# Performance work log

Hardware: AMD Instinct MI355X
Metric: run time of the kernel (lower is better)

## Reference

```python
import jax, jax.numpy as jnp
import numpy as np

EPS = 1e-5

def _layer_norm(x, gamma, beta):
    mu = jnp.mean(x, axis=-1, keepdims=True)
    var = jnp.var(x, axis=-1, keepdims=True)
    return (x - mu) * jax.lax.rsqrt(var + EPS) * gamma + beta

def setup_inputs() -> dict:
    key = jax.random.key(0)
    ks = jax.random.split(key, 4)
    B, T, D, H = 16, 2048, 1024, 1024
    s_in = 1.0 / np.sqrt(D)
    return {
        "x": jax.random.normal(ks[0], (B, T, D), dtype=jnp.float32),
        "c": jnp.zeros((B, H), dtype=jnp.float32),
        "W_lt": jax.random.uniform(ks[1], (H, D), jnp.float32, -s_in, s_in),
        "W_g": jax.random.uniform(ks[2], (2 * H, D), jnp.float32, -s_in, s_in),
        "b_g": jnp.zeros((2 * H,), dtype=jnp.float32),
        "gamma_g": jnp.ones((2 * H,), dtype=jnp.float32),
        "beta_g": jnp.zeros((2 * H,), dtype=jnp.float32),
        "gamma_a": jnp.ones((H,), dtype=jnp.float32),
        "beta_a": jnp.zeros((H,), dtype=jnp.float32),
    }

def reference(x, c, W_lt, W_g, b_g, gamma_g, beta_g, gamma_a, beta_a):
    H = W_lt.shape[0]
    # x: [B,T,D]
    x_tilde = jnp.einsum("btd,hd->bth", x, W_lt)            # [B,T,H]
    gate = jax.nn.sigmoid(_layer_norm(jnp.einsum("btd,gd->btg", x, W_g) + b_g, gamma_g, beta_g))
    f = gate[:, :, :H]                                        # forget gate [B,T,H]
    r = gate[:, :, H:]                                        # reset gate  [B,T,H]
    new_data = (1.0 - f) * x_tilde

    def step(c_prev, ft_nd):
        f_t, nd_t = ft_nd
        c_t = f_t * c_prev + nd_t
        return c_t, c_t

    # scan over time: move T to leading axis
    c_final, all_c = jax.lax.scan(step, c, (jnp.swapaxes(f, 0, 1), jnp.swapaxes(new_data, 0, 1)))
    all_c = jnp.swapaxes(all_c, 0, 1)                         # [B,T,H]
    h = r * jax.nn.sigmoid(_layer_norm(all_c, gamma_a, beta_a)) + (1.0 - r) * x
    return (h, c_final)
```

## Files before the change

### kernel.cpp

```cpp
#include <hip/hip_runtime.h>
#include <stdint.h>

typedef unsigned short u16;
typedef u16 us8 __attribute__((ext_vector_type(8)));
typedef uint32_t u32x8 __attribute__((ext_vector_type(8)));
typedef __bf16 bf16x8 __attribute__((ext_vector_type(8)));
typedef float f32x4 __attribute__((ext_vector_type(4)));

#define BB 16
#define TT 2048
#define HH 1024
#define MM 32768
#define NN 3072
#define KK 1024
#define NT 16

__device__ __forceinline__ float b2f(u16 u) {
    union { uint32_t i; float f; } v; v.i = ((uint32_t)u) << 16; return v.f;
}
__device__ __forceinline__ u16 f2b(float f) {
    union { uint32_t i; float f; } v; v.f = f;
    uint32_t r = v.i + 0x7fffu + ((v.i >> 16) & 1u);
    return (u16)(r >> 16);
}
__device__ __forceinline__ float sigm(float z) {
    return 1.f / (1.f + __expf(-z));
}
__device__ __forceinline__ void load_lds16(const u16* g, u16* l) {
    __builtin_amdgcn_global_load_lds(
        (const __attribute__((address_space(1))) void*)g,
        (__attribute__((address_space(3))) void*)l, 16, 0, 0);
}
__device__ __forceinline__ f32x4 mf(bf16x8 a, bf16x8 b, f32x4 c) {
    return __builtin_amdgcn_mfma_f32_16x16x32_bf16(a, b, c, 0, 0, 0);
}
#define MEMBAR() asm volatile("" ::: "memory")

__global__ __launch_bounds__(256) void k_cvt(const float* __restrict__ x,
                                             const float* __restrict__ wlt,
                                             const float* __restrict__ wg,
                                             u16* __restrict__ xb,
                                             u16* __restrict__ wb) {
    long i = (long)(blockIdx.x * 256 + threadIdx.x) * 8;
    const float* s;
    u16* o;
    if (i < 33554432L) { s = x + i; o = xb + i; }
    else {
        long j = i - 33554432L;
        s = (j < 1048576L) ? (wlt + j) : (wg + (j - 1048576L));
        o = wb + j;
    }
    float4 a = *(const float4*)(s);
    float4 b = *(const float4*)(s + 4);
    us8 r;
    r[0] = f2b(a.x); r[1] = f2b(a.y); r[2] = f2b(a.z); r[3] = f2b(a.w);
    r[4] = f2b(b.x); r[5] = f2b(b.y); r[6] = f2b(b.z); r[7] = f2b(b.w);
    *(us8*)o = r;
}

__global__ __launch_bounds__(512, 2) void k_gemm(const u16* __restrict__ A,
                                                 const u16* __restrict__ W,
                                                 u16* __restrict__ Y) {
    __shared__ u16 As[2 * 16384];
    __shared__ u16 Bs[2 * 16384];
    const int tid = threadIdx.x;
    const int lane = tid & 63;
    const int w = tid >> 6;
    const int wm = w >> 2;
    const int wn = w & 3;
    const int q = lane >> 4;
    const int l16 = lane & 15;

    const unsigned bid = blockIdx.y * 12u + blockIdx.x;
    const unsigned sw = (bid & 7u) * 192u + (bid >> 3);
    const int by = sw / 12u;
    const int bx = sw % 12u;

    const int slog = ((tid & 7) ^ ((tid >> 3) & 7)) << 3;
    const u16* aS = A + (size_t)(by * 256 + (tid >> 3)) * KK + slog;
    const u16* bS = W + (size_t)(bx * 256 + ((tid >> 8) << 6) + ((tid >> 3) & 31)) * KK + slog;
    u16* aD = As + w * 512;
    u16* bD = Bs + w * 512;

    load_lds16(aS,                aD);
    load_lds16(aS + 128 * KK,     aD + 4096);
    load_lds16(aS + 64 * KK,      aD + 8192);
    load_lds16(aS + 192 * KK,     aD + 12288);
    load_lds16(bS,                bD);
    load_lds16(bS + 128 * KK,     bD + 4096);
    load_lds16(bS + 32 * KK,      bD + 8192);
    load_lds16(bS + 160 * KK,     bD + 12288);
    load_lds16(aS + 64,           aD + 16384);
    load_lds16(aS + 64 + 128*KK,  aD + 16384 + 4096);
    load_lds16(aS + 64 + 64*KK,   aD + 16384 + 8192);
    load_lds16(aS + 64 + 192*KK,  aD + 16384 + 12288);
    load_lds16(bS + 64,           bD + 16384);
    load_lds16(bS + 64 + 128*KK,  bD + 16384 + 4096);
    load_lds16(bS + 64 + 32*KK,   bD + 16384 + 8192);
    load_lds16(bS + 64 + 160*KK,  bD + 16384 + 12288);

    const int key = l16 & 7;
    const int sA0 = ((q ^ key) << 3);
    const int sA1 = (((q ^ key) ^ 4) << 3);
    const int aB0 = wm * 4096 + l16 * 64 + sA0;
    const int aB1 = wm * 4096 + l16 * 64 + sA1;
    const int bB0 = wn * 2048 + l16 * 64 + sA0;
    const int bB1 = wn * 2048 + l16 * 64 + sA1;

    f32x4 zero = {0.f, 0.f, 0.f, 0.f};
    f32x4 acc[8][4];
#pragma unroll
    for (int i = 0; i < 8; ++i)
#pragma unroll
        for (int j = 0; j < 4; ++j) acc[i][j] = zero;
    bf16x8 aX[4], aY[4], bLo[4], bHi[4];

    asm volatile("s_waitcnt vmcnt(8)" ::: "memory");
    __builtin_amdgcn_sched_barrier(0);
    __builtin_amdgcn_s_barrier();
    MEMBAR();

    for (int kt = 0; kt < NT - 1; ++kt) {
        const int cb = (kt & 1) << 14;
        const int kc = (kt + 2) << 6;
        const bool st = (kt < NT - 2);
#pragma unroll
        for (int i = 0; i < 4; ++i) {
            aX[i] = *(const bf16x8*)&As[cb + i * 1024 + aB0];
            aY[i] = *(const bf16x8*)&As[cb + i * 1024 + aB1];
        }
        bLo[0] = *(const bf16x8*)&Bs[cb + bB0];
        bLo[1] = *(const bf16x8*)&Bs[cb + bB1];
        bLo[2] = *(const bf16x8*)&Bs[cb + 1024 + bB0];
        bLo[3] = *(const bf16x8*)&Bs[cb + 1024 + bB1];
        asm volatile("s_waitcnt lgkmcnt(8)" ::: "memory");
        __builtin_amdgcn_sched_barrier(0);
        __builtin_amdgcn_s_barrier();
        asm volatile("s_waitcnt lgkmcnt(0)" ::: "memory");
        __builtin_amdgcn_sched_barrier(0);
        __builtin_amdgcn_s_setprio(1);
#pragma unroll
        for (int i = 0; i < 4; ++i) {
            acc[i][0] = mf(aX[i], bLo[0], acc[i][0]);
            acc[i][0] = mf(aY[i], bLo[1], acc[i][0]);
            acc[i][1] = mf(aX[i], bLo[2], acc[i][1]);
            acc[i][1] = mf(aY[i], bLo[3], acc[i][1]);
        }
        __builtin_amdgcn_s_setprio(0);
        MEMBAR();
        __builtin_amdgcn_s_barrier();
        MEMBAR();
        bHi[0] = *(const bf16x8*)&Bs[cb + 8192 + bB0];
        bHi[1] = *(const bf16x8*)&Bs[cb + 8192 + bB1];
        bHi[2] = *(const bf16x8*)&Bs[cb + 8192 + 1024 + bB0];
        bHi[3] = *(const bf16x8*)&Bs[cb + 8192 + 1024 + bB1];
        if (st) {
            load_lds16(aS + kc,            aD + cb);
            load_lds16(aS + kc + 128*KK,   aD + cb + 4096);
            load_lds16(bS + kc,            bD + cb);
            load_lds16(bS + kc + 128*KK,   bD + cb + 4096);
        }
        __builtin_amdgcn_sched_barrier(0);
        __builtin_amdgcn_s_barrier();
        asm volatile("s_waitcnt lgkmcnt(0)" ::: "memory");
        __builtin_amdgcn_sched_barrier(0);
        __builtin_amdgcn_s_setprio(1);
#pragma unroll
        for (int i = 0; i < 4; ++i) {
            acc[i][2] = mf(aX[i], bHi[0], acc[i][2]);
            acc[i][2] = mf(aY[i], bHi[1], acc[i][2]);
            acc[i][3] = mf(aX[i], bHi[2], acc[i][3]);
            acc[i][3] = mf(aY[i], bHi[3], acc[i][3]);
        }
        __builtin_amdgcn_s_setprio(0);
        MEMBAR();
        __builtin_amdgcn_s_barrier();
        MEMBAR();
#pragma unroll
        for (int i = 0; i < 4; ++i) {
            aX[i] = *(const bf16x8*)&As[cb + 8192 + i * 1024 + aB0];
            aY[i] = *(const bf16x8*)&As[cb + 8192 + i * 1024 + aB1];
        }
        if (st) {
            load_lds16(bS + kc + 32*KK,    bD + cb + 8192);
            load_lds16(bS + kc + 160*KK,   bD + cb + 12288);
        }
        __builtin_amdgcn_sched_barrier(0);
        __builtin_amdgcn_s_barrier();
        asm volatile("s_waitcnt lgkmcnt(0)" ::: "memory");
        __builtin_amdgcn_sched_barrier(0);
        __builtin_amdgcn_s_setprio(1);
#pragma unroll
        for (int i = 0; i < 4; ++i) {
            acc[4 + i][0] = mf(aX[i], bLo[0], acc[4 + i][0]);
            acc[4 + i][0] = mf(aY[i], bLo[1], acc[4 + i][0]);
            acc[4 + i][1] = mf(aX[i], bLo[2], acc[4 + i][1]);
            acc[4 + i][1] = mf(aY[i], bLo[3], acc[4 + i][1]);
        }
        __builtin_amdgcn_s_setprio(0);
        MEMBAR();
        __builtin_amdgcn_s_barrier();
        MEMBAR();
        if (st) {
            load_lds16(aS + kc + 64*KK,    aD + cb + 8192);
            load_lds16(aS + kc + 192*KK,   aD + cb + 12288);
        }
        __builtin_amdgcn_sched_barrier(0);
        __builtin_amdgcn_s_barrier();
        __builtin_amdgcn_s_setprio(1);
#pragma unroll
        for (int i = 0; i < 4; ++i) {
            acc[4 + i][2] = mf(aX[i], bHi[0], acc[4 + i][2]);
            acc[4 + i][2] = mf(aY[i], bHi[1], acc[4 + i][2]);
            acc[4 + i][3] = mf(aX[i], bHi[2], acc[4 + i][3]);
            acc[4 + i][3] = mf(aY[i], bHi[3], acc[4 + i][3]);
        }
        __builtin_amdgcn_s_setprio(0);
        if (st) { asm volatile("s_waitcnt vmcnt(8)" ::: "memory"); }
        else    { asm volatile("s_waitcnt vmcnt(0)" ::: "memory"); }
        __builtin_amdgcn_sched_barrier(0);
        __builtin_amdgcn_s_barrier();
        MEMBAR();
    }

    {
        const int cb = 16384;
#pragma unroll
        for (int i = 0; i < 4; ++i) {
            aX[i] = *(const bf16x8*)&As[cb + i * 1024 + aB0];
            aY[i] = *(const bf16x8*)&As[cb + i * 1024 + aB1];
        }
        bLo[0] = *(const bf16x8*)&Bs[cb + bB0];
        bLo[1] = *(const bf16x8*)&Bs[cb + bB1];
        bLo[2] = *(const bf16x8*)&Bs[cb + 1024 + bB0];
        bLo[3] = *(const bf16x8*)&Bs[cb + 1024 + bB1];
        bHi[0] = *(const bf16x8*)&Bs[cb + 8192 + bB0];
        bHi[1] = *(const bf16x8*)&Bs[cb + 8192 + bB1];
        bHi[2] = *(const bf16x8*)&Bs[cb + 8192 + 1024 + bB0];
        bHi[3] = *(const bf16x8*)&Bs[cb + 8192 + 1024 + bB1];
#pragma unroll
        for (int i = 0; i < 4; ++i) {
            acc[i][0] = mf(aX[i], bLo[0], acc[i][0]);
            acc[i][0] = mf(aY[i], bLo[1], acc[i][0]);
            acc[i][1] = mf(aX[i], bLo[2], acc[i][1]);
            acc[i][1] = mf(aY[i], bLo[3], acc[i][1]);
            acc[i][2] = mf(aX[i], bHi[0], acc[i][2]);
            acc[i][2] = mf(aY[i], bHi[1], acc[i][2]);
            acc[i][3] = mf(aX[i], bHi[2], acc[i][3]);
            acc[i][3] = mf(aY[i], bHi[3], acc[i][3]);
        }
#pragma unroll
        for (int i = 0; i < 4; ++i) {
            aX[i] = *(const bf16x8*)&As[cb + 8192 + i * 1024 + aB0];
            aY[i] = *(const bf16x8*)&As[cb + 8192 + i * 1024 + aB1];
        }
#pragma unroll
        for (int i = 0; i < 4; ++i) {
            acc[4 + i][0] = mf(aX[i], bLo[0], acc[4 + i][0]);
            acc[4 + i][0] = mf(aY[i], bLo[1], acc[4 + i][0]);
            acc[4 + i][1] = mf(aX[i], bLo[2], acc[4 + i][1]);
            acc[4 + i][1] = mf(aY[i], bLo[3], acc[4 + i][1]);
            acc[4 + i][2] = mf(aX[i], bHi[0], acc[4 + i][2]);
            acc[4 + i][2] = mf(aY[i], bHi[1], acc[4 + i][2]);
            acc[4 + i][3] = mf(aX[i], bHi[2], acc[4 + i][3]);
            acc[4 + i][3] = mf(aY[i], bHi[3], acc[4 + i][3]);
        }
    }

#pragma unroll
    for (int fm = 0; fm < 8; ++fm) {
#pragma unroll
        for (int rg = 0; rg < 4; ++rg) {
            const int row = by * 256 + wm * 128 + fm * 16 + q * 4 + rg;
            u16* yp = Y + (size_t)row * NN + bx * 256 + wn * 64 + l16;
#pragma unroll
            for (int fn = 0; fn < 4; ++fn) yp[fn * 16] = f2b(acc[fm][fn][rg]);
        }
    }
}

__global__ __launch_bounds__(256) void k_lnsig(const u16* __restrict__ Y,
                                               const float* __restrict__ bg,
                                               const float* __restrict__ gg,
                                               const float* __restrict__ bt,
                                               uint32_t* __restrict__ FN,
                                               u16* __restrict__ R) {
    const int row = blockIdx.x;
    const int t = threadIdx.x;
    const u16* yr = Y + (size_t)row * 3072;
    us8 gv = *(const us8*)(yr + 1024 + t * 8);
    us8 xt;
    if (t < 128) xt = *(const us8*)(yr + t * 8);
    float z[8];
    float s = 0.f, s2 = 0.f;
#pragma unroll
    for (int k = 0; k < 8; k++) {
        z[k] = b2f(gv[k]) + bg[t * 8 + k];
        s += z[k];
        s2 += z[k] * z[k];
    }
#pragma unroll
    for (int m = 1; m < 64; m <<= 1) {
        s += __shfl_xor(s, m);
        s2 += __shfl_xor(s2, m);
    }
    __shared__ float red[8];
    if ((t & 63) == 0) { red[t >> 6] = s; red[(t >> 6) + 4] = s2; }
    asm volatile("s_waitcnt lgkmcnt(0)" ::: "memory");
    __builtin_amdgcn_sched_barrier(0);
    __builtin_amdgcn_s_barrier();
    MEMBAR();
    s = red[0] + red[1] + red[2] + red[3];
    s2 = red[4] + red[5] + red[6] + red[7];
    const float mu = s * (1.f / 2048.f);
    const float inv = rsqrtf(s2 * (1.f / 2048.f) - mu * mu + 1e-5f);
    float gate[8];
#pragma unroll
    for (int k = 0; k < 8; k++)
        gate[k] = sigm((z[k] - mu) * inv * gg[t * 8 + k] + bt[t * 8 + k]);
    if (t < 128) {
        u32x8 fn;
#pragma unroll
        for (int k = 0; k < 8; k++) {
            u16 fb = f2b(gate[k]);
            u16 nb = f2b((1.f - gate[k]) * b2f(xt[k]));
            fn[k] = (uint32_t)fb | ((uint32_t)nb << 16);
        }
        *(u32x8*)(FN + (size_t)row * 1024 + t * 8) = fn;
    } else {
        us8 ro;
#pragma unroll
        for (int k = 0; k < 8; k++) ro[k] = f2b(gate[k]);
        *(us8*)(R + (size_t)row * 1024 + (t - 128) * 8) = ro;
    }
}

__global__ __launch_bounds__(256) void k_scan1(const uint32_t* __restrict__ FN,
                                               float2* __restrict__ agg) {
    int u = blockIdx.x * 256 + threadIdx.x;
    int h2 = u & 511;
    int chunk = (u >> 9) & 31;
    int b = u >> 14;
    size_t base = (size_t)(b * 2048 + chunk * 64) * 1024 + h2 * 2;
    float F0 = 1.f, N0 = 0.f, F1 = 1.f, N1 = 0.f;
#pragma unroll 8
    for (int i = 0; i < 64; i++) {
        uint2 v = *(const uint2*)(FN + base + (size_t)i * 1024);
        float f0 = b2f((u16)(v.x & 0xffffu)), n0 = b2f((u16)(v.x >> 16));
        float f1 = b2f((u16)(v.y & 0xffffu)), n1 = b2f((u16)(v.y >> 16));
        N0 = fmaf(f0, N0, n0); F0 *= f0;
        N1 = fmaf(f1, N1, n1); F1 *= f1;
    }
    float4 o = {F0, N0, F1, N1};
    *(float4*)&agg[(size_t)(b * 32 + chunk) * 1024 + h2 * 2] = o;
}

__global__ __launch_bounds__(256) void k_scan2(const float2* __restrict__ agg,
                                               const float* __restrict__ c0,
                                               float* __restrict__ P) {
    int u = blockIdx.x * 256 + threadIdx.x;
    int b = u >> 10, h = u & 1023;
    float c = c0[u];
#pragma unroll 8
    for (int k = 0; k < 32; k++) {
        size_t idx = (size_t)(b * 32 + k) * 1024 + h;
        P[idx] = c;
        float2 fn = agg[idx];
        c = fmaf(fn.x, c, fn.y);
    }
}

#define SOUT_STEP(fnv, rvv, xvv, ro, p)                                        \
    {                                                                          \
        c0 = fmaf(b2f((u16)((fnv).x & 0xffffu)), c0, b2f((u16)((fnv).x >> 16)));\
        c1 = fmaf(b2f((u16)((fnv).y & 0xffffu)), c1, b2f((u16)((fnv).y >> 16)));\
        float s = c0 + c1, s2 = c0 * c0 + c1 * c1;                             \
        _Pragma("unroll")                                                      \
        for (int m = 1; m < 64; m <<= 1) {                                     \
            s += __shfl_xor(s, m);                                             \
            s2 += __shfl_xor(s2, m);                                           \
        }                                                                      \
        if (lane == 0) red[p][w] = make_float2(s, s2);                         \
        asm volatile("s_waitcnt lgkmcnt(0)" ::: "memory");                     \
        __builtin_amdgcn_sched_barrier(0);                                     \
        __builtin_amdgcn_s_barrier();                                          \
        MEMBAR();                                                              \
        s = 0.f; s2 = 0.f;                                                     \
        _Pragma("unroll")                                                      \
        for (int k = 0; k < 8; k++) { float2 v = red[p][k]; s += v.x; s2 += v.y; } \
        const float mu = s * (1.f / 1024.f);                                   \
        const float inv = rsqrtf(s2 * (1.f / 1024.f) - mu * mu + 1e-5f);       \
        const float sg0 = sigm((c0 - mu) * inv * g0 + be0);                    \
        const float sg1 = sigm((c1 - mu) * inv * g1 + be1);                    \
        const float r0 = b2f((u16)((rvv) & 0xffffu)), r1 = b2f((u16)((rvv) >> 16)); \
        const float x0 = b2f((u16)((xvv) & 0xffffu)), x1 = b2f((u16)((xvv) >> 16)); \
        float2 ho = {r0 * sg0 + (1.f - r0) * x0, r1 * sg1 + (1.f - r1) * x1};  \
        *(float2*)(out + (ro)) = ho;                                           \
    }

__global__ __launch_bounds__(512) void k_scanout(const uint32_t* __restrict__ FN,
                                                 const float* __restrict__ P,
                                                 const u16* __restrict__ R,
                                                 const u16* __restrict__ xb,
                                                 const float* __restrict__ ga,
                                                 const float* __restrict__ ba,
                                                 float* __restrict__ out,
                                                 float* __restrict__ cfin) {
    __shared__ float2 red[2][8];
    const int t = threadIdx.x;
    const int b = blockIdx.x >> 5, chunk = blockIdx.x & 31;
    const int h = t * 2;
    const int w = t >> 6, lane = t & 63;
    float2 cp = *(const float2*)&P[(size_t)(b * 32 + chunk) * 1024 + h];
    float c0 = cp.x, c1 = cp.y;
    const float g0 = ga[h], g1 = ga[h + 1];
    const float be0 = ba[h], be1 = ba[h + 1];
    const size_t base = (size_t)(b * 2048 + chunk * 64) * 1024 + h;

    uint2 fnA = *(const uint2*)(FN + base);
    uint32_t rvA = *(const uint32_t*)(R + base);
    uint32_t xvA = *(const uint32_t*)(xb + base);
    uint2 fnB = *(const uint2*)(FN + base + 1024);
    uint32_t rvB = *(const uint32_t*)(R + base + 1024);
    uint32_t xvB = *(const uint32_t*)(xb + base + 1024);

    for (int ii = 0; ii < 32; ++ii) {
        const size_t ro0 = base + (size_t)(2 * ii) * 1024;
        {
            uint2 fn = fnA; uint32_t rv = rvA, xv = xvA;
            if (ii < 31) {
                const size_t rn = ro0 + 2048;
                fnA = *(const uint2*)(FN + rn);
                rvA = *(const uint32_t*)(R + rn);
                xvA = *(const uint32_t*)(xb + rn);
            }
            SOUT_STEP(fn, rv, xv, ro0, 0)
        }
        {
            uint2 fn = fnB; uint32_t rv = rvB, xv = xvB;
            if (ii < 31) {
                const size_t rn = ro0 + 3072;
                fnB = *(const uint2*)(FN + rn);
                rvB = *(const uint32_t*)(R + rn);
                xvB = *(const uint32_t*)(xb + rn);
            }
            SOUT_STEP(fn, rv, xv, ro0 + 1024, 1)
        }
    }
    if (chunk == 31) *(float2*)(cfin + b * 1024 + h) = make_float2(c0, c1);
}

extern "C" void kernel_launch(void* const* d_in, const int* in_sizes, int n_in,
                              void* d_out, int out_size, void* d_ws, size_t ws_size,
                              hipStream_t stream) {
    const float* x   = (const float*)d_in[0];
    const float* c0  = (const float*)d_in[1];
    const float* wlt = (const float*)d_in[2];
    const float* wg  = (const float*)d_in[3];
    const float* bg  = (const float*)d_in[4];
    const float* gg  = (const float*)d_in[5];
    const float* btg = (const float*)d_in[6];
    const float* ga  = (const float*)d_in[7];
    const float* ba  = (const float*)d_in[8];
    float* out = (float*)d_out;

    char* ws = (char*)d_ws;
    u16* xb      = (u16*)(ws);
    u16* wb      = (u16*)(ws + 67108864);
    u16* y       = (u16*)(ws + 73400320);
    uint32_t* FN = (uint32_t*)(ws + 274726912);
    u16* R       = (u16*)(ws + 408944640);
    float2* agg  = (float2*)(ws + 476053504);
    float* P     = (float*)(ws + 480247808);

    k_cvt<<<17920, 256, 0, stream>>>(x, wlt, wg, xb, wb);
    k_gemm<<<dim3(NN / 256, MM / 256), 512, 0, stream>>>(xb, wb, y);
    k_lnsig<<<32768, 256, 0, stream>>>(y, bg, gg, btg, FN, R);
    k_scan1<<<1024, 256, 0, stream>>>(FN, agg);
    k_scan2<<<64, 256, 0, stream>>>(agg, c0, P);
    k_scanout<<<512, 512, 0, stream>>>(FN, P, R, xb, ga, ba, out,
                                       out + (size_t)33554432);
}
```

Baseline: 632.3 us.

## Make layernorm and scan-output kernels wave-per-row and shorten scan chunks

The LN+sigmoid kernel now gives each 64-lane wave a full row, so it no longer needs the shared-memory block reduction and barrier. The scan is split into 128 chunks of 16 steps instead of 32 chunks of 64. The output kernel has each wave own one (batch, chunk) unit across all 1024 channels, which removes the per-timestep block barrier and leaves only wave shuffles. Agg and P move to reuse the dead GEMM output region, and k_scan2 now runs a longer serial chain of 128 steps.

```diff
diff --git a/kernel.cpp b/kernel.cpp
--- a/kernel.cpp
+++ b/kernel.cpp
@@ -285,53 +285,64 @@
                                                const float* __restrict__ bt,
                                                uint32_t* __restrict__ FN,
                                                u16* __restrict__ R) {
-    const int row = blockIdx.x;
-    const int t = threadIdx.x;
+    const int lane = threadIdx.x & 63;
+    const int row = blockIdx.x * 4 + (threadIdx.x >> 6);
     const u16* yr = Y + (size_t)row * 3072;
-    us8 gv = *(const us8*)(yr + 1024 + t * 8);
-    us8 xt;
-    if (t < 128) xt = *(const us8*)(yr + t * 8);
-    float z[8];
+    const int g0i = 8 * lane;
+    us8 gv[4];
+    us8 xt[2];
+#pragma unroll
+    for (int j = 0; j < 4; ++j) gv[j] = *(const us8*)(yr + 1024 + g0i + 512 * j);
+#pragma unroll
+    for (int j = 0; j < 2; ++j) xt[j] = *(const us8*)(yr + g0i + 512 * j);
+    float z[4][8];
     float s = 0.f, s2 = 0.f;
 #pragma unroll
-    for (int k = 0; k < 8; k++) {
-        z[k] = b2f(gv[k]) + bg[t * 8 + k];
-        s += z[k];
-        s2 += z[k] * z[k];
+    for (int j = 0; j < 4; ++j) {
+        const float4 ba_ = *(const float4*)(bg + g0i + 512 * j);
+        const float4 bb_ = *(const float4*)(bg + g0i + 512 * j + 4);
+#pragma unroll
+        for (int k = 0; k < 4; ++k) {
+            z[j][k]     = b2f(gv[j][k])     + ((const float*)&ba_)[k];
+            z[j][k + 4] = b2f(gv[j][k + 4]) + ((const float*)&bb_)[k];
+        }
+#pragma unroll
+        for (int k = 0; k < 8; ++k) { s += z[j][k]; s2 = fmaf(z[j][k], z[j][k], s2); }
     }
 #pragma unroll
     for (int m = 1; m < 64; m <<= 1) {
         s += __shfl_xor(s, m);
         s2 += __shfl_xor(s2, m);
     }
-    __shared__ float red[8];
-    if ((t & 63) == 0) { red[t >> 6] = s; red[(t >> 6) + 4] = s2; }
-    asm volatile("s_waitcnt lgkmcnt(0)" ::: "memory");
-    __builtin_amdgcn_sched_barrier(0);
-    __builtin_amdgcn_s_barrier();
-    MEMBAR();
-    s = red[0] + red[1] + red[2] + red[3];
-    s2 = red[4] + red[5] + red[6] + red[7];
     const float mu = s * (1.f / 2048.f);
     const float inv = rsqrtf(s2 * (1.f / 2048.f) - mu * mu + 1e-5f);
-    float gate[8];
-#pragma unroll
-    for (int k = 0; k < 8; k++)
-        gate[k] = sigm((z[k] - mu) * inv * gg[t * 8 + k] + bt[t * 8 + k]);
-    if (t < 128) {
-        u32x8 fn;
-#pragma unroll
-        for (int k = 0; k < 8; k++) {
-            u16 fb = f2b(gate[k]);
-            u16 nb = f2b((1.f - gate[k]) * b2f(xt[k]));
-            fn[k] = (uint32_t)fb | ((uint32_t)nb << 16);
-        }
-        *(u32x8*)(FN + (size_t)row * 1024 + t * 8) = fn;
-    } else {
-        us8 ro;
-#pragma unroll
-        for (int k = 0; k < 8; k++) ro[k] = f2b(gate[k]);
-        *(us8*)(R + (size_t)row * 1024 + (t - 128) * 8) = ro;
+#pragma unroll
+    for (int j = 0; j < 4; ++j) {
+        const float4 ga_ = *(const float4*)(gg + g0i + 512 * j);
+        const float4 gb_ = *(const float4*)(gg + g0i + 512 * j + 4);
+        const float4 ta_ = *(const float4*)(bt + g0i + 512 * j);
+        const float4 tb_ = *(const float4*)(bt + g0i + 512 * j + 4);
+        float gate[8];
+#pragma unroll
+        for (int k = 0; k < 4; ++k) {
+            gate[k]     = sigm((z[j][k] - mu) * inv * ((const float*)&ga_)[k] + ((const float*)&ta_)[k]);
+            gate[k + 4] = sigm((z[j][k + 4] - mu) * inv * ((const float*)&gb_)[k] + ((const float*)&tb_)[k]);
+        }
+        if (j < 2) {
+            u32x8 fn;
+#pragma unroll
+            for (int k = 0; k < 8; ++k) {
+                u16 fb = f2b(gate[k]);
+                u16 nb = f2b((1.f - gate[k]) * b2f(xt[j][k]));
+                fn[k] = (uint32_t)fb | ((uint32_t)nb << 16);
+            }
+            *(u32x8*)(FN + (size_t)row * 1024 + g0i + 512 * j) = fn;
+        } else {
+            us8 ro;
+#pragma unroll
+            for (int k = 0; k < 8; ++k) ro[k] = f2b(gate[k]);
+            *(us8*)(R + (size_t)row * 1024 + g0i + 512 * (j - 2)) = ro;
+        }
     }
 }
 
@@ -339,12 +350,12 @@
                                                float2* __restrict__ agg) {
     int u = blockIdx.x * 256 + threadIdx.x;
     int h2 = u & 511;
-    int chunk = (u >> 9) & 31;
-    int b = u >> 14;
-    size_t base = (size_t)(b * 2048 + chunk * 64) * 1024 + h2 * 2;
+    int chunk = (u >> 9) & 127;
+    int b = u >> 16;
+    size_t base = (size_t)(b * 2048 + chunk * 16) * 1024 + h2 * 2;
     float F0 = 1.f, N0 = 0.f, F1 = 1.f, N1 = 0.f;
-#pragma unroll 8
-    for (int i = 0; i < 64; i++) {
+#pragma unroll
+    for (int i = 0; i < 16; i++) {
         uint2 v = *(const uint2*)(FN + base + (size_t)i * 1024);
         float f0 = b2f((u16)(v.x & 0xffffu)), n0 = b2f((u16)(v.x >> 16));
         float f1 = b2f((u16)(v.y & 0xffffu)), n1 = b2f((u16)(v.y >> 16));
@@ -352,7 +363,7 @@
         N1 = fmaf(f1, N1, n1); F1 *= f1;
     }
     float4 o = {F0, N0, F1, N1};
-    *(float4*)&agg[(size_t)(b * 32 + chunk) * 1024 + h2 * 2] = o;
+    *(float4*)&agg[(size_t)(b * 128 + chunk) * 1024 + h2 * 2] = o;
 }
 
 __global__ __launch_bounds__(256) void k_scan2(const float2* __restrict__ agg,
@@ -361,44 +372,16 @@
     int u = blockIdx.x * 256 + threadIdx.x;
     int b = u >> 10, h = u & 1023;
     float c = c0[u];
-#pragma unroll 8
-    for (int k = 0; k < 32; k++) {
-        size_t idx = (size_t)(b * 32 + k) * 1024 + h;
+#pragma unroll 4
+    for (int k = 0; k < 128; k++) {
+        size_t idx = (size_t)(b * 128 + k) * 1024 + h;
         P[idx] = c;
         float2 fn = agg[idx];
         c = fmaf(fn.x, c, fn.y);
     }
 }
 
-#define SOUT_STEP(fnv, rvv, xvv, ro, p)                                        \
-    {                                                                          \
-        c0 = fmaf(b2f((u16)((fnv).x & 0xffffu)), c0, b2f((u16)((fnv).x >> 16)));\
-        c1 = fmaf(b2f((u16)((fnv).y & 0xffffu)), c1, b2f((u16)((fnv).y >> 16)));\
-        float s = c0 + c1, s2 = c0 * c0 + c1 * c1;                             \
-        _Pragma("unroll")                                                      \
-        for (int m = 1; m < 64; m <<= 1) {                                     \
-            s += __shfl_xor(s, m);                                             \
-            s2 += __shfl_xor(s2, m);                                           \
-        }                                                                      \
-        if (lane == 0) red[p][w] = make_float2(s, s2);                         \
-        asm volatile("s_waitcnt lgkmcnt(0)" ::: "memory");                     \
-        __builtin_amdgcn_sched_barrier(0);                                     \
-        __builtin_amdgcn_s_barrier();                                          \
-        MEMBAR();                                                              \
-        s = 0.f; s2 = 0.f;                                                     \
-        _Pragma("unroll")                                                      \
-        for (int k = 0; k < 8; k++) { float2 v = red[p][k]; s += v.x; s2 += v.y; } \
-        const float mu = s * (1.f / 1024.f);                                   \
-        const float inv = rsqrtf(s2 * (1.f / 1024.f) - mu * mu + 1e-5f);       \
-        const float sg0 = sigm((c0 - mu) * inv * g0 + be0);                    \
-        const float sg1 = sigm((c1 - mu) * inv * g1 + be1);                    \
-        const float r0 = b2f((u16)((rvv) & 0xffffu)), r1 = b2f((u16)((rvv) >> 16)); \
-        const float x0 = b2f((u16)((xvv) & 0xffffu)), x1 = b2f((u16)((xvv) >> 16)); \
-        float2 ho = {r0 * sg0 + (1.f - r0) * x0, r1 * sg1 + (1.f - r1) * x1};  \
-        *(float2*)(out + (ro)) = ho;                                           \
-    }
-
-__global__ __launch_bounds__(512) void k_scanout(const uint32_t* __restrict__ FN,
+__global__ __launch_bounds__(256) void k_scanout(const uint32_t* __restrict__ FN,
                                                  const float* __restrict__ P,
                                                  const u16* __restrict__ R,
                                                  const u16* __restrict__ xb,
@@ -406,48 +389,63 @@
                                                  const float* __restrict__ ba,
                                                  float* __restrict__ out,
                                                  float* __restrict__ cfin) {
-    __shared__ float2 red[2][8];
-    const int t = threadIdx.x;
-    const int b = blockIdx.x >> 5, chunk = blockIdx.x & 31;
-    const int h = t * 2;
-    const int w = t >> 6, lane = t & 63;
-    float2 cp = *(const float2*)&P[(size_t)(b * 32 + chunk) * 1024 + h];
-    float c0 = cp.x, c1 = cp.y;
-    const float g0 = ga[h], g1 = ga[h + 1];
-    const float be0 = ba[h], be1 = ba[h + 1];
-    const size_t base = (size_t)(b * 2048 + chunk * 64) * 1024 + h;
-
-    uint2 fnA = *(const uint2*)(FN + base);
-    uint32_t rvA = *(const uint32_t*)(R + base);
-    uint32_t xvA = *(const uint32_t*)(xb + base);
-    uint2 fnB = *(const uint2*)(FN + base + 1024);
-    uint32_t rvB = *(const uint32_t*)(R + base + 1024);
-    uint32_t xvB = *(const uint32_t*)(xb + base + 1024);
-
-    for (int ii = 0; ii < 32; ++ii) {
-        const size_t ro0 = base + (size_t)(2 * ii) * 1024;
-        {
-            uint2 fn = fnA; uint32_t rv = rvA, xv = xvA;
-            if (ii < 31) {
-                const size_t rn = ro0 + 2048;
-                fnA = *(const uint2*)(FN + rn);
-                rvA = *(const uint32_t*)(R + rn);
-                xvA = *(const uint32_t*)(xb + rn);
-            }
-            SOUT_STEP(fn, rv, xv, ro0, 0)
-        }
-        {
-            uint2 fn = fnB; uint32_t rv = rvB, xv = xvB;
-            if (ii < 31) {
-                const size_t rn = ro0 + 3072;
-                fnB = *(const uint2*)(FN + rn);
-                rvB = *(const uint32_t*)(R + rn);
-                xvB = *(const uint32_t*)(xb + rn);
-            }
-            SOUT_STEP(fn, rv, xv, ro0 + 1024, 1)
-        }
-    }
-    if (chunk == 31) *(float2*)(cfin + b * 1024 + h) = make_float2(c0, c1);
+    const int lane = threadIdx.x & 63;
+    const int unit = blockIdx.x * 4 + (threadIdx.x >> 6);
+    const int b = unit >> 7, chunk = unit & 127;
+    float c0[8], c1[8], gg0[8], gg1[8], bb0[8], bb1[8];
+    const size_t pb = (size_t)(b * 128 + chunk) * 1024 + 2 * lane;
+#pragma unroll
+    for (int j = 0; j < 8; ++j) {
+        float2 cp = *(const float2*)&P[pb + 128 * j];
+        c0[j] = cp.x; c1[j] = cp.y;
+        float2 gv = *(const float2*)&ga[2 * lane + 128 * j];
+        gg0[j] = gv.x; gg1[j] = gv.y;
+        float2 bv = *(const float2*)&ba[2 * lane + 128 * j];
+        bb0[j] = bv.x; bb1[j] = bv.y;
+    }
+    const size_t base = (size_t)(b * 2048 + chunk * 16) * 1024 + 2 * lane;
+#pragma unroll 2
+    for (int i = 0; i < 16; ++i) {
+        const size_t ro = base + (size_t)i * 1024;
+        uint2 fn[8];
+        uint32_t rv[8], xv[8];
+#pragma unroll
+        for (int j = 0; j < 8; ++j) {
+            fn[j] = *(const uint2*)(FN + ro + 128 * j);
+            rv[j] = *(const uint32_t*)(R + ro + 128 * j);
+            xv[j] = *(const uint32_t*)(xb + ro + 128 * j);
+        }
+        float s = 0.f, s2 = 0.f;
+#pragma unroll
+        for (int j = 0; j < 8; ++j) {
+            c0[j] = fmaf(b2f((u16)(fn[j].x & 0xffffu)), c0[j], b2f((u16)(fn[j].x >> 16)));
+            c1[j] = fmaf(b2f((u16)(fn[j].y & 0xffffu)), c1[j], b2f((u16)(fn[j].y >> 16)));
+            s += c0[j] + c1[j];
+            s2 = fmaf(c0[j], c0[j], s2);
+            s2 = fmaf(c1[j], c1[j], s2);
+        }
+#pragma unroll
+        for (int m = 1; m < 64; m <<= 1) {
+            s += __shfl_xor(s, m);
+            s2 += __shfl_xor(s2, m);
+        }
+        const float mu = s * (1.f / 1024.f);
+        const float inv = rsqrtf(s2 * (1.f / 1024.f) - mu * mu + 1e-5f);
+#pragma unroll
+        for (int j = 0; j < 8; ++j) {
+            const float sg0 = sigm((c0[j] - mu) * inv * gg0[j] + bb0[j]);
+            const float sg1 = sigm((c1[j] - mu) * inv * gg1[j] + bb1[j]);
+            const float r0 = b2f((u16)(rv[j] & 0xffffu)), r1 = b2f((u16)(rv[j] >> 16));
+            const float x0 = b2f((u16)(xv[j] & 0xffffu)), x1 = b2f((u16)(xv[j] >> 16));
+            float2 ho = {r0 * sg0 + (1.f - r0) * x0, r1 * sg1 + (1.f - r1) * x1};
+            *(float2*)(out + ro + 128 * j) = ho;
+        }
+    }
+    if (chunk == 127) {
+#pragma unroll
+        for (int j = 0; j < 8; ++j)
+            *(float2*)(cfin + b * 1024 + 2 * lane + 128 * j) = make_float2(c0[j], c1[j]);
+    }
 }
 
 extern "C" void kernel_launch(void* const* d_in, const int* in_sizes, int n_in,
@@ -470,14 +468,14 @@
     u16* y       = (u16*)(ws + 73400320);
     uint32_t* FN = (uint32_t*)(ws + 274726912);
     u16* R       = (u16*)(ws + 408944640);
-    float2* agg  = (float2*)(ws + 476053504);
-    float* P     = (float*)(ws + 480247808);
+    float2* agg  = (float2*)(ws + 73400320);
+    float* P     = (float*)(ws + 73400320 + 16777216);
 
     k_cvt<<<17920, 256, 0, stream>>>(x, wlt, wg, xb, wb);
     k_gemm<<<dim3(NN / 256, MM / 256), 512, 0, stream>>>(xb, wb, y);
-    k_lnsig<<<32768, 256, 0, stream>>>(y, bg, gg, btg, FN, R);
-    k_scan1<<<1024, 256, 0, stream>>>(FN, agg);
+    k_lnsig<<<8192, 256, 0, stream>>>(y, bg, gg, btg, FN, R);
+    k_scan1<<<4096, 256, 0, stream>>>(FN, agg);
     k_scan2<<<64, 256, 0, stream>>>(agg, c0, P);
-    k_scanout<<<512, 512, 0, stream>>>(FN, P, R, xb, ga, ba, out,
+    k_scanout<<<512, 256, 0, stream>>>(FN, P, R, xb, ga, ba, out,
                                        out + (size_t)33554432);
 }
```

After: 674.3 us. +6.6%, slower.

## Fold chunk-prefix scan into scanout and widen scan1 loads

Applied to the files above, without the earlier changes.

Removes the separate k_scan2 kernel that sequentially combined chunk aggregates into per-chunk carry-in values. Each k_scanout block now recomputes its own carry-in by folding the aggregates of all preceding chunks. k_scan1 also processes four hidden units per thread with 16-byte loads and launches half as many blocks. This saves one launch and a small serial kernel, but adds redundant prefix work of up to 31 steps per block in scanout.

```diff
diff --git a/kernel.cpp b/kernel.cpp
--- a/kernel.cpp
+++ b/kernel.cpp
@@ -338,36 +338,29 @@
 __global__ __launch_bounds__(256) void k_scan1(const uint32_t* __restrict__ FN,
                                                float2* __restrict__ agg) {
     int u = blockIdx.x * 256 + threadIdx.x;
-    int h2 = u & 511;
-    int chunk = (u >> 9) & 31;
-    int b = u >> 14;
-    size_t base = (size_t)(b * 2048 + chunk * 64) * 1024 + h2 * 2;
+    int h4 = u & 255;
+    int chunk = (u >> 8) & 31;
+    int b = u >> 13;
+    size_t base = (size_t)(b * 2048 + chunk * 64) * 1024 + h4 * 4;
     float F0 = 1.f, N0 = 0.f, F1 = 1.f, N1 = 0.f;
+    float F2 = 1.f, N2 = 0.f, F3 = 1.f, N3 = 0.f;
 #pragma unroll 8
     for (int i = 0; i < 64; i++) {
-        uint2 v = *(const uint2*)(FN + base + (size_t)i * 1024);
+        uint4 v = *(const uint4*)(FN + base + (size_t)i * 1024);
         float f0 = b2f((u16)(v.x & 0xffffu)), n0 = b2f((u16)(v.x >> 16));
         float f1 = b2f((u16)(v.y & 0xffffu)), n1 = b2f((u16)(v.y >> 16));
+        float f2 = b2f((u16)(v.z & 0xffffu)), n2 = b2f((u16)(v.z >> 16));
+        float f3 = b2f((u16)(v.w & 0xffffu)), n3 = b2f((u16)(v.w >> 16));
         N0 = fmaf(f0, N0, n0); F0 *= f0;
         N1 = fmaf(f1, N1, n1); F1 *= f1;
-    }
-    float4 o = {F0, N0, F1, N1};
-    *(float4*)&agg[(size_t)(b * 32 + chunk) * 1024 + h2 * 2] = o;
-}
-
-__global__ __launch_bounds__(256) void k_scan2(const float2* __restrict__ agg,
-                                               const float* __restrict__ c0,
-                                               float* __restrict__ P) {
-    int u = blockIdx.x * 256 + threadIdx.x;
-    int b = u >> 10, h = u & 1023;
-    float c = c0[u];
-#pragma unroll 8
-    for (int k = 0; k < 32; k++) {
-        size_t idx = (size_t)(b * 32 + k) * 1024 + h;
-        P[idx] = c;
-        float2 fn = agg[idx];
-        c = fmaf(fn.x, c, fn.y);
-    }
+        N2 = fmaf(f2, N2, n2); F2 *= f2;
+        N3 = fmaf(f3, N3, n3); F3 *= f3;
+    }
+    size_t oi = (size_t)(b * 32 + chunk) * 1024 + h4 * 4;
+    float4 oA = {F0, N0, F1, N1};
+    float4 oB = {F2, N2, F3, N3};
+    *(float4*)&agg[oi] = oA;
+    *(float4*)&agg[oi + 2] = oB;
 }
 
 #define SOUT_STEP(fnv, rvv, xvv, ro, p)                                        \
@@ -399,7 +392,8 @@
     }
 
 __global__ __launch_bounds__(512) void k_scanout(const uint32_t* __restrict__ FN,
-                                                 const float* __restrict__ P,
+                                                 const float2* __restrict__ agg,
+                                                 const float* __restrict__ cin,
                                                  const u16* __restrict__ R,
                                                  const u16* __restrict__ xb,
                                                  const float* __restrict__ ga,
@@ -411,8 +405,15 @@
     const int b = blockIdx.x >> 5, chunk = blockIdx.x & 31;
     const int h = t * 2;
     const int w = t >> 6, lane = t & 63;
-    float2 cp = *(const float2*)&P[(size_t)(b * 32 + chunk) * 1024 + h];
+
+    float2 cp = *(const float2*)&cin[b * 1024 + h];
     float c0 = cp.x, c1 = cp.y;
+    for (int k = 0; k < chunk; ++k) {
+        float4 a4 = *(const float4*)&agg[(size_t)(b * 32 + k) * 1024 + h];
+        c0 = fmaf(a4.x, c0, a4.y);
+        c1 = fmaf(a4.z, c1, a4.w);
+    }
+
     const float g0 = ga[h], g1 = ga[h + 1];
     const float be0 = ba[h], be1 = ba[h + 1];
     const size_t base = (size_t)(b * 2048 + chunk * 64) * 1024 + h;
@@ -471,13 +472,11 @@
     uint32_t* FN = (uint32_t*)(ws + 274726912);
     u16* R       = (u16*)(ws + 408944640);
     float2* agg  = (float2*)(ws + 476053504);
-    float* P     = (float*)(ws + 480247808);
 
     k_cvt<<<17920, 256, 0, stream>>>(x, wlt, wg, xb, wb);
     k_gemm<<<dim3(NN / 256, MM / 256), 512, 0, stream>>>(xb, wb, y);
     k_lnsig<<<32768, 256, 0, stream>>>(y, bg, gg, btg, FN, R);
-    k_scan1<<<1024, 256, 0, stream>>>(FN, agg);
-    k_scan2<<<64, 256, 0, stream>>>(agg, c0, P);
-    k_scanout<<<512, 512, 0, stream>>>(FN, P, R, xb, ga, ba, out,
+    k_scan1<<<512, 256, 0, stream>>>(FN, agg);
+    k_scanout<<<512, 512, 0, stream>>>(FN, agg, c0, R, xb, ga, ba, out,
                                        out + (size_t)33554432);
 }
```

Result: no change. 634.7 us (+0.4%).
